# Optimization experiments

Measured on AMD Instinct MI355X. Metric: run time of the kernel, lower is better.

The kernel has to match this reference:

```python
import jax, jax.numpy as jnp
import numpy as np

N = 200_000        # total nodes
E = 6_400_000      # total edges (avg degree 32)
G = 2_000          # number of graphs in the batch
IN_DIM = 128
LAT = 32           # each GCN layer width
HID = 128

def _glorot(key, shape):
    fan_in, fan_out = shape[0], shape[1]
    s = jnp.sqrt(2.0 / (fan_in + fan_out)).astype(jnp.float32)
    return jax.random.normal(key, shape, dtype=jnp.float32) * s

def setup_inputs() -> dict:
    key = jax.random.key(0)
    ks = jax.random.split(key, 8)
    x = jax.random.normal(ks[0], (N, IN_DIM), dtype=jnp.float32)
    edge_index = jax.random.randint(ks[1], (2, E), 0, N, dtype=jnp.int32)
    # sorted batch assignment with every graph id present (PyG-style contiguous graphs)
    batch = ((jnp.arange(N, dtype=jnp.int32) * G) // N).astype(jnp.int32)
    return {
        "x": x,
        "edge_index": edge_index,
        "batch": batch,
        "W1": _glorot(ks[2], (IN_DIM, LAT)), "b1": jnp.zeros((LAT,), jnp.float32),
        "W2": _glorot(ks[3], (LAT, LAT)),    "b2": jnp.zeros((LAT,), jnp.float32),
        "W3": _glorot(ks[4], (LAT, LAT)),    "b3": jnp.zeros((LAT,), jnp.float32),
        "Wl1": _glorot(ks[5], (3 * LAT, HID)), "bl1": jnp.zeros((HID,), jnp.float32),
        "Wl2": _glorot(ks[6], (HID, 2)),       "bl2": jnp.zeros((2,), jnp.float32),
    }

def reference(x, edge_index, batch, W1, b1, W2, b2, W3, b3, Wl1, bl1, Wl2, bl2):
    n = x.shape[0]
    src, dst = edge_index[0], edge_index[1]
    loops = jnp.arange(n, dtype=src.dtype)
    src_f = jnp.concatenate([src, loops])  # add self-loops (GCNConv default)
    dst_f = jnp.concatenate([dst, loops])
    # symmetric normalization deg^{-1/2}[src] * deg^{-1/2}[dst]
    deg = jax.ops.segment_sum(jnp.ones((src_f.shape[0],), x.dtype), dst_f, num_segments=n)
    dinv = jnp.where(deg > 0, jax.lax.rsqrt(jnp.maximum(deg, 1e-12)), 0.0)
    norm = dinv[src_f] * dinv[dst_f]  # [E+N]

    def gcn(h, W, b):
        h = h @ W                                  # transform BEFORE propagate (PyG GCNConv)
        msg = h[src_f] * norm[:, None]             # gather + scale, [E+N, LAT]
        agg = jax.ops.segment_sum(msg, dst_f, num_segments=n)
        return jnp.tanh(agg + b)

    h1 = gcn(x, W1, b1)
    h2 = gcn(h1, W2, b2)
    h3 = gcn(h2, W3, b3)
    hcat = jnp.concatenate([h1, h2, h3], axis=1)   # [N, 96]

    # readout: first node of each graph (torch.nonzero(batch==i)[0] on sorted batch)
    idx = jnp.searchsorted(batch, jnp.arange(G, dtype=batch.dtype))
    pooled = hcat[idx]                              # [G, 96]

    hidden = jax.nn.relu(pooled @ Wl1 + bl1)
    logits = jax.nn.log_softmax(hidden @ Wl2 + bl2, axis=1)  # [G, 2]
    return logits
```

## Files before the change

### kernel.cpp

```cpp
#include <hip/hip_runtime.h>
#include <hip/hip_bf16.h>
#include <math.h>

#define IN_DIM 128
#define LAT 32
#define HID 128
#define RSHIFT 8
#define RANGE 256
#define KMAX 1024
#define PART_CH 12288
#define PART_T 1024
#define CAP 9216
#define GIN_ROWS 32
#define LCAP 128

typedef unsigned short u16;

__device__ __forceinline__ float bf2f(u16 v) {
    return __uint_as_float(((unsigned int)v) << 16);
}
__device__ __forceinline__ u16 f2bf(float f) {
    unsigned int u = __float_as_uint(f);
    u += 0x7fff + ((u >> 16) & 1);
    return (u16)(u >> 16);
}


__global__ void pmap_kernel(const int* __restrict__ batch, int* __restrict__ pmap, int N) {
    int v = blockIdx.x * blockDim.x + threadIdx.x;
    if (v >= N) return;
    int b = batch[v];
    int prev = (v == 0) ? -1 : batch[v - 1];
    pmap[v] = (b != prev) ? (b + 1) : 0;
}

__global__ void compute_idx_kernel(const int* __restrict__ batch, int* __restrict__ idx,
                                   int N, int G) {
    int g = blockIdx.x * blockDim.x + threadIdx.x;
    if (g >= G) return;
    int lo = 0, hi = N;
    while (lo < hi) {
        int mid = (lo + hi) >> 1;
        if (batch[mid] < g) lo = mid + 1; else hi = mid;
    }
    idx[g] = lo;
}

__global__ void init_cursor_kernel(int* __restrict__ bucketCursor, int K) {
    int b = blockIdx.x * blockDim.x + threadIdx.x;
    if (b < K) bucketCursor[b] = b * CAP;
}


__global__ void partition_kernel(const int* __restrict__ ei, int* __restrict__ bucketCursor,
                                 unsigned int* __restrict__ pairs, long long E, int K) {
    __shared__ unsigned int stage[PART_CH];
    __shared__ int histS[KMAX];
    __shared__ int curS[KMAX];
    __shared__ int gbase[KMAX];
    __shared__ int ssum[PART_T];
    int t = threadIdx.x;
    if (t < KMAX) histS[t] = 0;
    __syncthreads();
    long long e0 = (long long)blockIdx.x * PART_CH;
    int cnt = (int)min((long long)PART_CH, E - e0);
    for (int i = t; i < cnt; i += PART_T) {
        int d = ei[E + e0 + i];
        atomicAdd(&histS[d >> RSHIFT], 1);
    }
    __syncthreads();
    int h = (t < K) ? histS[t] : 0;
    if (t < K) gbase[t] = h ? atomicAdd(&bucketCursor[t], h) : 0;
    ssum[t] = h;
    __syncthreads();
    for (int off = 1; off < PART_T; off <<= 1) {
        int v = (t >= off) ? ssum[t - off] : 0;
        __syncthreads();
        ssum[t] += v;
        __syncthreads();
    }
    int excl = ssum[t] - h;
    if (t < KMAX) { histS[t] = excl; curS[t] = excl; }
    __syncthreads();
    for (int i = t; i < cnt; i += PART_T) {
        long long e = e0 + i;
        unsigned int s = (unsigned int)ei[e];
        int d = ei[E + e];
        int b = d >> RSHIFT;
        int p = atomicAdd(&curS[b], 1);
        stage[p] = (s << RSHIFT) | (unsigned int)(d & (RANGE - 1));
    }
    __syncthreads();
    for (int i = t; i < cnt; i += PART_T) {
        int lo = 0, hi = K - 1;
        while (lo < hi) {
            int mid = (lo + hi + 1) >> 1;
            if (histS[mid] <= i) lo = mid; else hi = mid - 1;
        }
        pairs[(long long)gbase[lo] + (i - histS[lo])] = stage[i];
    }
}

__global__ void post_scan_kernel(const int* __restrict__ bucketCursor, int* __restrict__ bucketStart,
                                 int K, int Etot, int* __restrict__ rowptr, int N) {
    __shared__ int s[KMAX];
    int t = threadIdx.x;
    int c = (t < K) ? (bucketCursor[t] - t * CAP) : 0;
    s[t] = c;
    __syncthreads();
    for (int off = 1; off < KMAX; off <<= 1) {
        int v = (t >= off) ? s[t - off] : 0;
        __syncthreads();
        s[t] += v;
        __syncthreads();
    }
    if (t < K) bucketStart[t] = s[t] - c;
    if (t == 0) {
        bucketStart[K] = Etot;
        rowptr[N] = Etot;
    }
}

__global__ void build_csr_kernel(const unsigned int* __restrict__ pairs,
                                 const int* __restrict__ bucketStart,
                                 int* __restrict__ rowptr, float* __restrict__ dinv,
                                 int* __restrict__ csr_src, int N) {
    __shared__ int hist[RANGE];
    __shared__ int scanb[RANGE];
    __shared__ int cursor[RANGE];
    int b = blockIdx.x;
    int t = threadIdx.x;
    int base = b << RSHIFT;
    int s0 = bucketStart[b];
    int cnt = bucketStart[b + 1] - s0;
    long long rbase = (long long)b * CAP;
    hist[t] = 0;
    __syncthreads();
    for (int i = t; i < cnt; i += RANGE) {
        unsigned int p = pairs[rbase + i];
        atomicAdd(&hist[p & (RANGE - 1)], 1);
    }
    __syncthreads();
    int deg = hist[t];
    scanb[t] = deg;
    __syncthreads();
    for (int off = 1; off < RANGE; off <<= 1) {
        int tmp = (t >= off) ? scanb[t - off] : 0;
        __syncthreads();
        scanb[t] += tmp;
        __syncthreads();
    }
    int excl = scanb[t] - deg;
    int node = base + t;
    if (node < N) {
        rowptr[node] = s0 + excl;
        dinv[node] = rsqrtf((float)(deg + 1));
    }
    cursor[t] = s0 + excl;
    __syncthreads();
    for (int i = t; i < cnt; i += RANGE) {
        unsigned int p = pairs[rbase + i];
        int slot = atomicAdd(&cursor[p & (RANGE - 1)], 1);
        csr_src[slot] = (int)(p >> RSHIFT);
    }
}


__global__ void rscan_kernel(const int* __restrict__ rowptr, const int* __restrict__ idx,
                             int* __restrict__ offs, int* __restrict__ totalT, int G) {
    __shared__ int s[256];
    int t = threadIdx.x;
    int per = (G + 255) / 256;
    int loc[16];
    int base = t * per;
    int sum = 0;
    for (int k = 0; k < per; k++) {
        int g = base + k;
        int c = 0;
        if (g < G) { int v = idx[g]; c = rowptr[v + 1] - rowptr[v] + 1; }
        loc[k] = sum; sum += c;
    }
    s[t] = sum;
    __syncthreads();
    for (int off = 1; off < 256; off <<= 1) {
        int v = (t >= off) ? s[t - off] : 0;
        __syncthreads();
        s[t] += v;
        __syncthreads();
    }
    int b0 = (t > 0) ? s[t - 1] : 0;
    for (int k = 0; k < per; k++) {
        int g = base + k;
        if (g < G) offs[g] = b0 + loc[k];
    }
    if (t == 255) totalT[0] = s[255];
}

__global__ void rfill_kernel(const int* __restrict__ rowptr, const int* __restrict__ csr_src,
                             const int* __restrict__ idx, const int* __restrict__ offs,
                             int* __restrict__ list, int G) {
    int g = blockIdx.x * 4 + (int)(threadIdx.x >> 6);
    int lane = threadIdx.x & 63;
    if (g >= G) return;
    int v = idx[g];
    int o = offs[g];
    int s0 = rowptr[v], s1 = rowptr[v + 1];
    if (lane == 0) list[o] = v;
    for (int i = lane; i < s1 - s0; i += 64) list[o + 1 + i] = csr_src[s0 + i];
}


__global__ void gemm_in_kernel(const float* __restrict__ x, const float* __restrict__ W,
                               const float* __restrict__ dinv, u16* __restrict__ tp, int N) {
    __shared__ float Wl[IN_DIM * LAT];
    __shared__ float Xl[GIN_ROWS * IN_DIM];
    int t = threadIdx.x;
    for (int i = t; i < IN_DIM * LAT; i += 256) Wl[i] = W[i];
    long long rowBase = (long long)blockIdx.x * GIN_ROWS;
    int nrow = min(GIN_ROWS, (int)(N - rowBase));
    {
        const float4* x4 = reinterpret_cast<const float4*>(x + rowBase * IN_DIM);
        float4* X4 = reinterpret_cast<float4*>(Xl);
        int nf4 = nrow * (IN_DIM / 4);
        for (int i = t; i < nf4; i += 256) X4[i] = x4[i];
    }
    __syncthreads();
    int g = t >> 5;
    int c = t & 31;
    int r0 = g * 4;
    float acc0 = 0.f, acc1 = 0.f, acc2 = 0.f, acc3 = 0.f;
#pragma unroll 4
    for (int k = 0; k < IN_DIM; k += 4) {
        float w0 = Wl[(k + 0) * LAT + c];
        float w1 = Wl[(k + 1) * LAT + c];
        float w2 = Wl[(k + 2) * LAT + c];
        float w3 = Wl[(k + 3) * LAT + c];
        float4 xa = *reinterpret_cast<const float4*>(&Xl[(r0 + 0) * IN_DIM + k]);
        float4 xb = *reinterpret_cast<const float4*>(&Xl[(r0 + 1) * IN_DIM + k]);
        float4 xc = *reinterpret_cast<const float4*>(&Xl[(r0 + 2) * IN_DIM + k]);
        float4 xd = *reinterpret_cast<const float4*>(&Xl[(r0 + 3) * IN_DIM + k]);
        acc0 += xa.x * w0 + xa.y * w1 + xa.z * w2 + xa.w * w3;
        acc1 += xb.x * w0 + xb.y * w1 + xb.z * w2 + xb.w * w3;
        acc2 += xc.x * w0 + xc.y * w1 + xc.z * w2 + xc.w * w3;
        acc3 += xd.x * w0 + xd.y * w1 + xd.z * w2 + xd.w * w3;
    }
    long long rr = rowBase + r0;
    if (r0 + 0 < nrow) tp[(rr + 0) * LAT + c] = f2bf(acc0 * dinv[rr + 0]);
    if (r0 + 1 < nrow) tp[(rr + 1) * LAT + c] = f2bf(acc1 * dinv[rr + 1]);
    if (r0 + 2 < nrow) tp[(rr + 2) * LAT + c] = f2bf(acc2 * dinv[rr + 2]);
    if (r0 + 3 < nrow) tp[(rr + 3) * LAT + c] = f2bf(acc3 * dinv[rr + 3]);
}


__global__ void gather_fused_kernel(const int* __restrict__ rowptr, const int* __restrict__ csr_src,
                                    const u16* __restrict__ tp, const float* __restrict__ dinv,
                                    const float* __restrict__ bcur, const int* __restrict__ pmap,
                                    float* __restrict__ pooled, int colOff,
                                    const float* __restrict__ Wnext, u16* __restrict__ tpNext,
                                    const int* __restrict__ vmap, const int* __restrict__ nvDev,
                                    int nvMax) {
    __shared__ float Wl[LAT * LAT];
    for (int i = threadIdx.x; i < LAT * LAT; i += blockDim.x) Wl[i] = Wnext[i];
    __syncthreads();
    int vi = blockIdx.x * 8 + (int)(threadIdx.x >> 5);
    int f = threadIdx.x & 31;
    int Nv = nvDev ? nvDev[0] : nvMax;
    if (vi >= Nv) return;
    int v = vmap ? vmap[vi] : vi;
    int start = rowptr[v];
    int end = rowptr[v + 1];
    float acc = bf2f(tp[(long long)v * LAT + f]);
    int e = start;
    for (; e + 32 <= end; e += 32) {
        int s = csr_src[e + f];
#pragma unroll
        for (int jj = 0; jj < 32; jj += 8) {
            int s0 = __shfl(s, jj + 0, 32), s1 = __shfl(s, jj + 1, 32);
            int s2 = __shfl(s, jj + 2, 32), s3 = __shfl(s, jj + 3, 32);
            int s4 = __shfl(s, jj + 4, 32), s5 = __shfl(s, jj + 5, 32);
            int s6 = __shfl(s, jj + 6, 32), s7 = __shfl(s, jj + 7, 32);
            float r0 = bf2f(tp[(long long)s0 * LAT + f]);
            float r1 = bf2f(tp[(long long)s1 * LAT + f]);
            float r2 = bf2f(tp[(long long)s2 * LAT + f]);
            float r3 = bf2f(tp[(long long)s3 * LAT + f]);
            float r4 = bf2f(tp[(long long)s4 * LAT + f]);
            float r5 = bf2f(tp[(long long)s5 * LAT + f]);
            float r6 = bf2f(tp[(long long)s6 * LAT + f]);
            float r7 = bf2f(tp[(long long)s7 * LAT + f]);
            acc += ((r0 + r1) + (r2 + r3)) + ((r4 + r5) + (r6 + r7));
        }
    }
    int rem = end - e;
    if (rem > 0) {
        int s = (f < rem) ? csr_src[e + f] : 0;
        int j = 0;
        for (; j + 4 <= rem; j += 4) {
            int s0 = __shfl(s, j + 0, 32), s1 = __shfl(s, j + 1, 32);
            int s2 = __shfl(s, j + 2, 32), s3 = __shfl(s, j + 3, 32);
            float r0 = bf2f(tp[(long long)s0 * LAT + f]);
            float r1 = bf2f(tp[(long long)s1 * LAT + f]);
            float r2 = bf2f(tp[(long long)s2 * LAT + f]);
            float r3 = bf2f(tp[(long long)s3 * LAT + f]);
            acc += (r0 + r1) + (r2 + r3);
        }
        for (; j < rem; j++) {
            int sj = __shfl(s, j, 32);
            acc += bf2f(tp[(long long)sj * LAT + f]);
        }
    }
    float dv = dinv[v];
    float hv = tanhf(dv * acc + bcur[f]);
    int pg = pmap[v];
    if (pg) pooled[(long long)(pg - 1) * (3 * LAT) + colOff + f] = hv;
    float acc2 = 0.f;
#pragma unroll
    for (int k = 0; k < LAT; k++) acc2 += __shfl(hv, k, 32) * Wl[k * LAT + f];
    tpNext[(long long)v * LAT + f] = f2bf(acc2 * dv);
}


__global__ void gather_readout_kernel(const int* __restrict__ rowptr, const int* __restrict__ csr_src,
                                      const u16* __restrict__ tp, const float* __restrict__ dinv,
                                      const float* __restrict__ bcur, const int* __restrict__ idx,
                                      float* __restrict__ pooled, int colOff, int G) {
    int vi = blockIdx.x * 8 + (int)(threadIdx.x >> 5);
    int f = threadIdx.x & 31;
    if (vi >= G) return;
    int v = idx[vi];
    int start = rowptr[v];
    int end = rowptr[v + 1];
    float acc = bf2f(tp[(long long)v * LAT + f]);
    int e = start;
    for (; e + 32 <= end; e += 32) {
        int s = csr_src[e + f];
#pragma unroll
        for (int jj = 0; jj < 32; jj += 8) {
            int s0 = __shfl(s, jj + 0, 32), s1 = __shfl(s, jj + 1, 32);
            int s2 = __shfl(s, jj + 2, 32), s3 = __shfl(s, jj + 3, 32);
            int s4 = __shfl(s, jj + 4, 32), s5 = __shfl(s, jj + 5, 32);
            int s6 = __shfl(s, jj + 6, 32), s7 = __shfl(s, jj + 7, 32);
            float r0 = bf2f(tp[(long long)s0 * LAT + f]);
            float r1 = bf2f(tp[(long long)s1 * LAT + f]);
            float r2 = bf2f(tp[(long long)s2 * LAT + f]);
            float r3 = bf2f(tp[(long long)s3 * LAT + f]);
            float r4 = bf2f(tp[(long long)s4 * LAT + f]);
            float r5 = bf2f(tp[(long long)s5 * LAT + f]);
            float r6 = bf2f(tp[(long long)s6 * LAT + f]);
            float r7 = bf2f(tp[(long long)s7 * LAT + f]);
            acc += ((r0 + r1) + (r2 + r3)) + ((r4 + r5) + (r6 + r7));
        }
    }
    int rem = end - e;
    if (rem > 0) {
        int s = (f < rem) ? csr_src[e + f] : 0;
        for (int j = 0; j < rem; j++) {
            int sj = __shfl(s, j, 32);
            acc += bf2f(tp[(long long)sj * LAT + f]);
        }
    }
    float hv = tanhf(dinv[v] * acc + bcur[f]);
    pooled[(long long)vi * (3 * LAT) + colOff + f] = hv;
}


__global__ void mlp_head_kernel(const float* __restrict__ pooled,
                                const float* __restrict__ Wl1, const float* __restrict__ bl1,
                                const float* __restrict__ Wl2, const float* __restrict__ bl2,
                                float* __restrict__ out, int G) {
    __shared__ float prow[3 * LAT];
    __shared__ float red0[HID];
    __shared__ float red1[HID];
    int g = blockIdx.x;
    int j = threadIdx.x;
    if (j < 3 * LAT) prow[j] = pooled[(long long)g * (3 * LAT) + j];
    __syncthreads();
    float acc = bl1[j];
#pragma unroll 8
    for (int k = 0; k < 3 * LAT; k++) acc += prow[k] * Wl1[k * HID + j];
    float hj = fmaxf(acc, 0.f);
    red0[j] = hj * Wl2[j * 2 + 0];
    red1[j] = hj * Wl2[j * 2 + 1];
    __syncthreads();
    for (int s = HID / 2; s > 0; s >>= 1) {
        if (j < s) { red0[j] += red0[j + s]; red1[j] += red1[j + s]; }
        __syncthreads();
    }
    if (j == 0) {
        float l0 = red0[0] + bl2[0];
        float l1 = red1[0] + bl2[1];
        float m = fmaxf(l0, l1);
        float lse = m + logf(expf(l0 - m) + expf(l1 - m));
        out[(long long)g * 2 + 0] = l0 - lse;
        out[(long long)g * 2 + 1] = l1 - lse;
    }
}


extern "C" void kernel_launch(void* const* d_in, const int* in_sizes, int n_in,
                              void* d_out, int out_size, void* d_ws, size_t ws_size,
                              hipStream_t stream) {
    const float* x    = (const float*)d_in[0];
    const int*   ei   = (const int*)d_in[1];
    const int*   batch= (const int*)d_in[2];
    const float* W1   = (const float*)d_in[3];
    const float* b1   = (const float*)d_in[4];
    const float* W2   = (const float*)d_in[5];
    const float* b2   = (const float*)d_in[6];
    const float* W3   = (const float*)d_in[7];
    const float* b3   = (const float*)d_in[8];
    const float* Wl1  = (const float*)d_in[9];
    const float* bl1  = (const float*)d_in[10];
    const float* Wl2  = (const float*)d_in[11];
    const float* bl2  = (const float*)d_in[12];
    float* out = (float*)d_out;

    const int N = in_sizes[2];
    const long long E = (long long)in_sizes[1] / 2;
    const int G = out_size / 2;
    const int K = (N + RANGE - 1) >> RSHIFT;
    const int capT = G * LCAP;

    char* ws = (char*)d_ws;
    size_t off = 0;
    char*  regionA = ws + off;           off += (size_t)K * CAP * 4;
    char*  bufB    = ws + off;           off += (size_t)N * LAT * 2;
    int*   csr_src = (int*)  (ws + off); off += (size_t)E * 4;
    float* dinv    = (float*)(ws + off); off += (size_t)N * 4;
    int*   rowptr  = (int*)  (ws + off); off += (size_t)(N + 1) * 4;
    int*   pmap    = (int*)  (ws + off); off += (size_t)N * 4;
    int*   idx     = (int*)  (ws + off); off += (size_t)G * 4;
    float* pooled  = (float*)(ws + off); off += (size_t)G * (3 * LAT) * 4;
    int*   bucketStart  = (int*)(ws + off); off += (KMAX + 1) * 4;
    int*   bucketCursor = (int*)(ws + off); off += KMAX * 4;
    int*   offs    = (int*)  (ws + off); off += (size_t)G * 4;
    int*   totalT  = (int*)  (ws + off); off += 4;
    int*   list    = (int*)  (ws + off); off += (size_t)capT * 4;

    unsigned int* pairs = (unsigned int*)regionA;
    u16* tpA = (u16*)regionA;
    u16* tpB = (u16*)bufB;

    const int BS = 256;
    const int gatherBlocks = (N + 7) / 8;
    const int g2Blocks = (capT + 7) / 8;
    const int groBlocks = (G + 7) / 8;
    const int ginBlocks = (N + GIN_ROWS - 1) / GIN_ROWS;
    const int partBlocks = (int)((E + PART_CH - 1) / PART_CH);

    pmap_kernel<<<(N + BS - 1) / BS, BS, 0, stream>>>(batch, pmap, N);
    compute_idx_kernel<<<(G + BS - 1) / BS, BS, 0, stream>>>(batch, idx, N, G);
    init_cursor_kernel<<<(K + BS - 1) / BS, BS, 0, stream>>>(bucketCursor, K);
    partition_kernel<<<partBlocks, PART_T, 0, stream>>>(ei, bucketCursor, pairs, E, K);
    post_scan_kernel<<<1, KMAX, 0, stream>>>(bucketCursor, bucketStart, K, (int)E, rowptr, N);
    build_csr_kernel<<<K, RANGE, 0, stream>>>(pairs, bucketStart, rowptr, dinv, csr_src, N);

    rscan_kernel<<<1, 256, 0, stream>>>(rowptr, idx, offs, totalT, G);
    rfill_kernel<<<(G + 3) / 4, BS, 0, stream>>>(rowptr, csr_src, idx, offs, list, G);

    gemm_in_kernel<<<ginBlocks, BS, 0, stream>>>(x, W1, dinv, tpA, N);

    gather_fused_kernel<<<gatherBlocks, BS, 0, stream>>>(rowptr, csr_src, tpA, dinv, b1, pmap,
                                                         pooled, 0, W2, tpB,
                                                         (const int*)nullptr, (const int*)nullptr, N);
    gather_fused_kernel<<<g2Blocks, BS, 0, stream>>>(rowptr, csr_src, tpB, dinv, b2, pmap,
                                                     pooled, LAT, W3, tpA,
                                                     list, totalT, capT);
    gather_readout_kernel<<<groBlocks, BS, 0, stream>>>(rowptr, csr_src, tpA, dinv, b3, idx,
                                                        pooled, 2 * LAT, G);

    mlp_head_kernel<<<G, HID, 0, stream>>>(pooled, Wl1, bl1, Wl2, bl2, out, G);
}
```

Before: 463.1 us.

## Tile GCN gathers by source-node range to keep feature rows L2-resident

```diff
diff --git a/kernel.cpp b/kernel.cpp
--- a/kernel.cpp
+++ b/kernel.cpp
@@ -12,7 +12,7 @@
 #define PART_T 1024
 #define CAP 9216
 #define GIN_ROWS 32
-#define LCAP 128
+#define LCAP 96
 
 typedef unsigned short u16;
 
@@ -23,6 +23,9 @@
     unsigned int u = __float_as_uint(f);
     u += 0x7fff + ((u >> 16) & 1);
     return (u16)(u >> 16);
+}
+__device__ __forceinline__ int tile_of(int src, int T) {
+    return (src >= 3 * T) ? 3 : (src >= 2 * T) ? 2 : (src >= T) ? 1 : 0;
 }
 
 
@@ -123,45 +126,56 @@
 
 __global__ void build_csr_kernel(const unsigned int* __restrict__ pairs,
                                  const int* __restrict__ bucketStart,
-                                 int* __restrict__ rowptr, float* __restrict__ dinv,
-                                 int* __restrict__ csr_src, int N) {
-    __shared__ int hist[RANGE];
-    __shared__ int scanb[RANGE];
-    __shared__ int cursor[RANGE];
+                                 int* __restrict__ rowptr, int4* __restrict__ r2,
+                                 float* __restrict__ dinv, int* __restrict__ csr_src,
+                                 int N, int T) {
+    __shared__ int hist[KMAX];
+    __shared__ int cursor[KMAX];
+    __shared__ int ssum[RANGE];
     int b = blockIdx.x;
     int t = threadIdx.x;
     int base = b << RSHIFT;
     int s0 = bucketStart[b];
     int cnt = bucketStart[b + 1] - s0;
     long long rbase = (long long)b * CAP;
-    hist[t] = 0;
+    for (int j = t; j < KMAX; j += RANGE) hist[j] = 0;
     __syncthreads();
     for (int i = t; i < cnt; i += RANGE) {
         unsigned int p = pairs[rbase + i];
-        atomicAdd(&hist[p & (RANGE - 1)], 1);
-    }
-    __syncthreads();
-    int deg = hist[t];
-    scanb[t] = deg;
+        int src = (int)(p >> RSHIFT);
+        int key = ((int)(p & (RANGE - 1)) << 2) | tile_of(src, T);
+        atomicAdd(&hist[key], 1);
+    }
+    __syncthreads();
+    int h0 = hist[4 * t + 0], h1 = hist[4 * t + 1],
+        h2 = hist[4 * t + 2], h3 = hist[4 * t + 3];
+    int deg = h0 + h1 + h2 + h3;
+    ssum[t] = deg;
     __syncthreads();
     for (int off = 1; off < RANGE; off <<= 1) {
-        int tmp = (t >= off) ? scanb[t - off] : 0;
-        __syncthreads();
-        scanb[t] += tmp;
-        __syncthreads();
-    }
-    int excl = scanb[t] - deg;
+        int v = (t >= off) ? ssum[t - off] : 0;
+        __syncthreads();
+        ssum[t] += v;
+        __syncthreads();
+    }
+    int kbase = s0 + ssum[t] - deg;
     int node = base + t;
     if (node < N) {
-        rowptr[node] = s0 + excl;
+        rowptr[node] = kbase;
+        r2[node] = make_int4(kbase, kbase + h0, kbase + h0 + h1, kbase + h0 + h1 + h2);
         dinv[node] = rsqrtf((float)(deg + 1));
     }
-    cursor[t] = s0 + excl;
+    cursor[4 * t + 0] = kbase;
+    cursor[4 * t + 1] = kbase + h0;
+    cursor[4 * t + 2] = kbase + h0 + h1;
+    cursor[4 * t + 3] = kbase + h0 + h1 + h2;
     __syncthreads();
     for (int i = t; i < cnt; i += RANGE) {
         unsigned int p = pairs[rbase + i];
-        int slot = atomicAdd(&cursor[p & (RANGE - 1)], 1);
-        csr_src[slot] = (int)(p >> RSHIFT);
+        int src = (int)(p >> RSHIFT);
+        int key = ((int)(p & (RANGE - 1)) << 2) | tile_of(src, T);
+        int slot = atomicAdd(&cursor[key], 1);
+        csr_src[slot] = src;
     }
 }
 
@@ -252,24 +266,22 @@
 }
 
 
-__global__ void gather_fused_kernel(const int* __restrict__ rowptr, const int* __restrict__ csr_src,
-                                    const u16* __restrict__ tp, const float* __restrict__ dinv,
-                                    const float* __restrict__ bcur, const int* __restrict__ pmap,
-                                    float* __restrict__ pooled, int colOff,
-                                    const float* __restrict__ Wnext, u16* __restrict__ tpNext,
-                                    const int* __restrict__ vmap, const int* __restrict__ nvDev,
-                                    int nvMax) {
-    __shared__ float Wl[LAT * LAT];
-    for (int i = threadIdx.x; i < LAT * LAT; i += blockDim.x) Wl[i] = Wnext[i];
-    __syncthreads();
+__global__ void gather_tile_kernel(const int* __restrict__ rowptr, const int4* __restrict__ r2,
+                                   const int* __restrict__ csr_src, const u16* __restrict__ tp,
+                                   _Float16* __restrict__ agg, int pass, int T,
+                                   const int* __restrict__ vmap, const int* __restrict__ nvDev,
+                                   int nvMax) {
+    int Nv = nvDev ? nvDev[0] : nvMax;
+    if (blockIdx.x * 8 >= Nv) return;
     int vi = blockIdx.x * 8 + (int)(threadIdx.x >> 5);
     int f = threadIdx.x & 31;
-    int Nv = nvDev ? nvDev[0] : nvMax;
     if (vi >= Nv) return;
     int v = vmap ? vmap[vi] : vi;
-    int start = rowptr[v];
-    int end = rowptr[v + 1];
-    float acc = bf2f(tp[(long long)v * LAT + f]);
+    int4 rr = r2[v];
+    int start = (pass == 0) ? rr.x : (pass == 1) ? rr.y : (pass == 2) ? rr.z : rr.w;
+    int end   = (pass == 0) ? rr.y : (pass == 1) ? rr.z : (pass == 2) ? rr.w : rowptr[v + 1];
+    float acc = 0.f;
+    if (tile_of(v, T) == pass) acc = bf2f(tp[(long long)v * LAT + f]);
     int e = start;
     for (; e + 32 <= end; e += 32) {
         int s = csr_src[e + f];
@@ -281,13 +293,13 @@
             int s6 = __shfl(s, jj + 6, 32), s7 = __shfl(s, jj + 7, 32);
             float r0 = bf2f(tp[(long long)s0 * LAT + f]);
             float r1 = bf2f(tp[(long long)s1 * LAT + f]);
-            float r2 = bf2f(tp[(long long)s2 * LAT + f]);
+            float r2_ = bf2f(tp[(long long)s2 * LAT + f]);
             float r3 = bf2f(tp[(long long)s3 * LAT + f]);
             float r4 = bf2f(tp[(long long)s4 * LAT + f]);
             float r5 = bf2f(tp[(long long)s5 * LAT + f]);
             float r6 = bf2f(tp[(long long)s6 * LAT + f]);
             float r7 = bf2f(tp[(long long)s7 * LAT + f]);
-            acc += ((r0 + r1) + (r2 + r3)) + ((r4 + r5) + (r6 + r7));
+            acc += ((r0 + r1) + (r2_ + r3)) + ((r4 + r5) + (r6 + r7));
         }
     }
     int rem = end - e;
@@ -299,17 +311,39 @@
             int s2 = __shfl(s, j + 2, 32), s3 = __shfl(s, j + 3, 32);
             float r0 = bf2f(tp[(long long)s0 * LAT + f]);
             float r1 = bf2f(tp[(long long)s1 * LAT + f]);
-            float r2 = bf2f(tp[(long long)s2 * LAT + f]);
+            float r2_ = bf2f(tp[(long long)s2 * LAT + f]);
             float r3 = bf2f(tp[(long long)s3 * LAT + f]);
-            acc += (r0 + r1) + (r2 + r3);
+            acc += (r0 + r1) + (r2_ + r3);
         }
         for (; j < rem; j++) {
             int sj = __shfl(s, j, 32);
             acc += bf2f(tp[(long long)sj * LAT + f]);
         }
     }
+    _Float16* ag = agg + (long long)vi * LAT + f;
+    if (pass == 0) *ag = (_Float16)acc;
+    else *ag = (_Float16)((float)*ag + acc);
+}
+
+
+__global__ void epilogue_kernel(const _Float16* __restrict__ agg, const float* __restrict__ dinv,
+                                const float* __restrict__ bcur, const int* __restrict__ pmap,
+                                float* __restrict__ pooled, int colOff,
+                                const float* __restrict__ Wnext, u16* __restrict__ tpNext,
+                                const int* __restrict__ vmap, const int* __restrict__ nvDev,
+                                int nvMax) {
+    int Nv = nvDev ? nvDev[0] : nvMax;
+    if (blockIdx.x * 8 >= Nv) return;
+    __shared__ float Wl[LAT * LAT];
+    for (int i = threadIdx.x; i < LAT * LAT; i += blockDim.x) Wl[i] = Wnext[i];
+    __syncthreads();
+    int vi = blockIdx.x * 8 + (int)(threadIdx.x >> 5);
+    int f = threadIdx.x & 31;
+    if (vi >= Nv) return;
+    int v = vmap ? vmap[vi] : vi;
+    float a = (float)agg[(long long)vi * LAT + f];
     float dv = dinv[v];
-    float hv = tanhf(dv * acc + bcur[f]);
+    float hv = tanhf(dv * a + bcur[f]);
     int pg = pmap[v];
     if (pg) pooled[(long long)(pg - 1) * (3 * LAT) + colOff + f] = hv;
     float acc2 = 0.f;
@@ -419,6 +453,7 @@
     const int G = out_size / 2;
     const int K = (N + RANGE - 1) >> RSHIFT;
     const int capT = G * LCAP;
+    const int T = (N + 3) / 4;
 
     char* ws = (char*)d_ws;
     size_t off = 0;
@@ -427,6 +462,7 @@
     int*   csr_src = (int*)  (ws + off); off += (size_t)E * 4;
     float* dinv    = (float*)(ws + off); off += (size_t)N * 4;
     int*   rowptr  = (int*)  (ws + off); off += (size_t)(N + 1) * 4;
+    int4*  r2      = (int4*) (ws + off); off += (size_t)N * 16;
     int*   pmap    = (int*)  (ws + off); off += (size_t)N * 4;
     int*   idx     = (int*)  (ws + off); off += (size_t)G * 4;
     float* pooled  = (float*)(ws + off); off += (size_t)G * (3 * LAT) * 4;
@@ -438,6 +474,7 @@
 
     unsigned int* pairs = (unsigned int*)regionA;
     u16* tpA = (u16*)regionA;
+    _Float16* agg = (_Float16*)(regionA + (size_t)N * LAT * 2);
     u16* tpB = (u16*)bufB;
 
     const int BS = 256;
@@ -452,19 +489,25 @@
     init_cursor_kernel<<<(K + BS - 1) / BS, BS, 0, stream>>>(bucketCursor, K);
     partition_kernel<<<partBlocks, PART_T, 0, stream>>>(ei, bucketCursor, pairs, E, K);
     post_scan_kernel<<<1, KMAX, 0, stream>>>(bucketCursor, bucketStart, K, (int)E, rowptr, N);
-    build_csr_kernel<<<K, RANGE, 0, stream>>>(pairs, bucketStart, rowptr, dinv, csr_src, N);
+    build_csr_kernel<<<K, RANGE, 0, stream>>>(pairs, bucketStart, rowptr, r2, dinv, csr_src, N, T);
 
     rscan_kernel<<<1, 256, 0, stream>>>(rowptr, idx, offs, totalT, G);
     rfill_kernel<<<(G + 3) / 4, BS, 0, stream>>>(rowptr, csr_src, idx, offs, list, G);
 
     gemm_in_kernel<<<ginBlocks, BS, 0, stream>>>(x, W1, dinv, tpA, N);
 
-    gather_fused_kernel<<<gatherBlocks, BS, 0, stream>>>(rowptr, csr_src, tpA, dinv, b1, pmap,
-                                                         pooled, 0, W2, tpB,
-                                                         (const int*)nullptr, (const int*)nullptr, N);
-    gather_fused_kernel<<<g2Blocks, BS, 0, stream>>>(rowptr, csr_src, tpB, dinv, b2, pmap,
-                                                     pooled, LAT, W3, tpA,
-                                                     list, totalT, capT);
+    for (int p = 0; p < 4; p++)
+        gather_tile_kernel<<<gatherBlocks, BS, 0, stream>>>(rowptr, r2, csr_src, tpA, agg, p, T,
+                                                            (const int*)nullptr, (const int*)nullptr, N);
+    epilogue_kernel<<<gatherBlocks, BS, 0, stream>>>(agg, dinv, b1, pmap, pooled, 0, W2, tpB,
+                                                     (const int*)nullptr, (const int*)nullptr, N);
+
+    for (int p = 0; p < 4; p++)
+        gather_tile_kernel<<<g2Blocks, BS, 0, stream>>>(rowptr, r2, csr_src, tpB, agg, p, T,
+                                                        list, totalT, capT);
+    epilogue_kernel<<<g2Blocks, BS, 0, stream>>>(agg, dinv, b2, pmap, pooled, LAT, W3, tpA,
+                                                 list, totalT, capT);
+
     gather_readout_kernel<<<groBlocks, BS, 0, stream>>>(rowptr, csr_src, tpA, dinv, b3, idx,
                                                         pooled, 2 * LAT, G);
 
```

Measured after the change: 596.5 us. 1.29x slower.

## Retile input GEMM to 2x4 register blocks with padded shared rows; early-exit idle gather blocks

Applied to the files above, without the earlier changes.

```diff
diff --git a/kernel.cpp b/kernel.cpp
--- a/kernel.cpp
+++ b/kernel.cpp
@@ -11,8 +11,9 @@
 #define PART_CH 12288
 #define PART_T 1024
 #define CAP 9216
-#define GIN_ROWS 32
-#define LCAP 128
+#define GIN_ROWS 64
+#define XPAD 132
+#define LCAP 96
 
 typedef unsigned short u16;
 
@@ -213,42 +214,55 @@
 __global__ void gemm_in_kernel(const float* __restrict__ x, const float* __restrict__ W,
                                const float* __restrict__ dinv, u16* __restrict__ tp, int N) {
     __shared__ float Wl[IN_DIM * LAT];
-    __shared__ float Xl[GIN_ROWS * IN_DIM];
+    __shared__ float Xl[GIN_ROWS * XPAD];
     int t = threadIdx.x;
-    for (int i = t; i < IN_DIM * LAT; i += 256) Wl[i] = W[i];
+    {
+        const float4* w4 = reinterpret_cast<const float4*>(W);
+        float4* W4 = reinterpret_cast<float4*>(Wl);
+        for (int i = t; i < IN_DIM * LAT / 4; i += 256) W4[i] = w4[i];
+    }
     long long rowBase = (long long)blockIdx.x * GIN_ROWS;
     int nrow = min(GIN_ROWS, (int)(N - rowBase));
     {
         const float4* x4 = reinterpret_cast<const float4*>(x + rowBase * IN_DIM);
-        float4* X4 = reinterpret_cast<float4*>(Xl);
-        int nf4 = nrow * (IN_DIM / 4);
-        for (int i = t; i < nf4; i += 256) X4[i] = x4[i];
-    }
-    __syncthreads();
-    int g = t >> 5;
-    int c = t & 31;
-    int r0 = g * 4;
-    float acc0 = 0.f, acc1 = 0.f, acc2 = 0.f, acc3 = 0.f;
+        for (int i = t; i < nrow * (IN_DIM / 4); i += 256) {
+            int r = i >> 5, kq = i & 31;
+            *reinterpret_cast<float4*>(&Xl[r * XPAD + kq * 4]) = x4[i];
+        }
+    }
+    __syncthreads();
+    int rp = t >> 3;
+    int c0 = (t & 7) * 4;
+    int r0 = 2 * rp, r1 = 2 * rp + 1;
+    float4 a0 = {0.f, 0.f, 0.f, 0.f};
+    float4 a1 = {0.f, 0.f, 0.f, 0.f};
 #pragma unroll 4
     for (int k = 0; k < IN_DIM; k += 4) {
-        float w0 = Wl[(k + 0) * LAT + c];
-        float w1 = Wl[(k + 1) * LAT + c];
-        float w2 = Wl[(k + 2) * LAT + c];
-        float w3 = Wl[(k + 3) * LAT + c];
-        float4 xa = *reinterpret_cast<const float4*>(&Xl[(r0 + 0) * IN_DIM + k]);
-        float4 xb = *reinterpret_cast<const float4*>(&Xl[(r0 + 1) * IN_DIM + k]);
-        float4 xc = *reinterpret_cast<const float4*>(&Xl[(r0 + 2) * IN_DIM + k]);
-        float4 xd = *reinterpret_cast<const float4*>(&Xl[(r0 + 3) * IN_DIM + k]);
-        acc0 += xa.x * w0 + xa.y * w1 + xa.z * w2 + xa.w * w3;
-        acc1 += xb.x * w0 + xb.y * w1 + xb.z * w2 + xb.w * w3;
-        acc2 += xc.x * w0 + xc.y * w1 + xc.z * w2 + xc.w * w3;
-        acc3 += xd.x * w0 + xd.y * w1 + xd.z * w2 + xd.w * w3;
-    }
-    long long rr = rowBase + r0;
-    if (r0 + 0 < nrow) tp[(rr + 0) * LAT + c] = f2bf(acc0 * dinv[rr + 0]);
-    if (r0 + 1 < nrow) tp[(rr + 1) * LAT + c] = f2bf(acc1 * dinv[rr + 1]);
-    if (r0 + 2 < nrow) tp[(rr + 2) * LAT + c] = f2bf(acc2 * dinv[rr + 2]);
-    if (r0 + 3 < nrow) tp[(rr + 3) * LAT + c] = f2bf(acc3 * dinv[rr + 3]);
+        float4 w0 = *reinterpret_cast<const float4*>(&Wl[(k + 0) * LAT + c0]);
+        float4 w1 = *reinterpret_cast<const float4*>(&Wl[(k + 1) * LAT + c0]);
+        float4 w2 = *reinterpret_cast<const float4*>(&Wl[(k + 2) * LAT + c0]);
+        float4 w3 = *reinterpret_cast<const float4*>(&Wl[(k + 3) * LAT + c0]);
+        float4 xa = *reinterpret_cast<const float4*>(&Xl[r0 * XPAD + k]);
+        float4 xb = *reinterpret_cast<const float4*>(&Xl[r1 * XPAD + k]);
+        a0.x += xa.x * w0.x + xa.y * w1.x + xa.z * w2.x + xa.w * w3.x;
+        a0.y += xa.x * w0.y + xa.y * w1.y + xa.z * w2.y + xa.w * w3.y;
+        a0.z += xa.x * w0.z + xa.y * w1.z + xa.z * w2.z + xa.w * w3.z;
+        a0.w += xa.x * w0.w + xa.y * w1.w + xa.z * w2.w + xa.w * w3.w;
+        a1.x += xb.x * w0.x + xb.y * w1.x + xb.z * w2.x + xb.w * w3.x;
+        a1.y += xb.x * w0.y + xb.y * w1.y + xb.z * w2.y + xb.w * w3.y;
+        a1.z += xb.x * w0.z + xb.y * w1.z + xb.z * w2.z + xb.w * w3.z;
+        a1.w += xb.x * w0.w + xb.y * w1.w + xb.z * w2.w + xb.w * w3.w;
+    }
+    if (r0 < nrow) {
+        float dv = dinv[rowBase + r0];
+        ushort4 o = { f2bf(a0.x * dv), f2bf(a0.y * dv), f2bf(a0.z * dv), f2bf(a0.w * dv) };
+        *reinterpret_cast<ushort4*>(&tp[(rowBase + r0) * LAT + c0]) = o;
+    }
+    if (r1 < nrow) {
+        float dv = dinv[rowBase + r1];
+        ushort4 o = { f2bf(a1.x * dv), f2bf(a1.y * dv), f2bf(a1.z * dv), f2bf(a1.w * dv) };
+        *reinterpret_cast<ushort4*>(&tp[(rowBase + r1) * LAT + c0]) = o;
+    }
 }
 
 
@@ -259,12 +273,13 @@
                                     const float* __restrict__ Wnext, u16* __restrict__ tpNext,
                                     const int* __restrict__ vmap, const int* __restrict__ nvDev,
                                     int nvMax) {
+    int Nv = nvDev ? nvDev[0] : nvMax;
+    if (blockIdx.x * 8 >= Nv) return;
     __shared__ float Wl[LAT * LAT];
     for (int i = threadIdx.x; i < LAT * LAT; i += blockDim.x) Wl[i] = Wnext[i];
     __syncthreads();
     int vi = blockIdx.x * 8 + (int)(threadIdx.x >> 5);
     int f = threadIdx.x & 31;
-    int Nv = nvDev ? nvDev[0] : nvMax;
     if (vi >= Nv) return;
     int v = vmap ? vmap[vi] : vi;
     int start = rowptr[v];
```

Result: faster. 440.5 us (-4.9%).
